# Kernel tuning notes

Measured on AMD Instinct MI355X. Metric: run time of the kernel, lower is better.

Reference implementation:

```python
import jax, jax.numpy as jnp
import numpy as np

EMBED_DIM = 1024
NUM_HEADS = 16
HEAD_DIM = EMBED_DIM // NUM_HEADS


def setup_inputs() -> dict:
    key = jax.random.key(0)
    kx, kq, kk, kv, ko = jax.random.split(key, 5)
    B, S = 4, 2048
    std = 1.0 / np.sqrt(EMBED_DIM)
    x = jax.random.normal(kx, (B, S, EMBED_DIM), dtype=jnp.float32)
    # nn.Linear weights stored as [out, in]; applied as x @ W.T
    Wq = jax.random.normal(kq, (EMBED_DIM, EMBED_DIM), dtype=jnp.float32) * std
    Wk = jax.random.normal(kk, (EMBED_DIM, EMBED_DIM), dtype=jnp.float32) * std
    Wv = jax.random.normal(kv, (EMBED_DIM, EMBED_DIM), dtype=jnp.float32) * std
    Wo = jax.random.normal(ko, (EMBED_DIM, EMBED_DIM), dtype=jnp.float32) * std
    return {"x": x, "Wq": Wq, "Wk": Wk, "Wv": Wv, "Wo": Wo}


def reference(x, Wq, Wk, Wv, Wo):
    B, S, E = x.shape
    H, D = NUM_HEADS, HEAD_DIM
    scale = jnp.sqrt(jnp.float32(D))

    def proj(W):
        # x @ W.T -> (B, S, E) -> (B, H, S, D)
        return (x @ W.T).reshape(B, S, H, D).transpose(0, 2, 1, 3)

    q, k, v = proj(Wq), proj(Wk), proj(Wv)
    scores = jnp.einsum("bhsd,bhtd->bhst", q, k) / scale  # (B,H,S,S)
    causal = jnp.tril(jnp.ones((S, S), dtype=bool))
    scores = jnp.where(causal, scores, -jnp.inf)
    attn = jax.nn.softmax(scores, axis=-1)  # dropout in eval mode = identity
    out = jnp.einsum("bhst,bhtd->bhsd", attn, v)  # (B,H,S,D)
    out = out.transpose(0, 2, 1, 3).reshape(B, S, E)
    return out @ Wo.T
```

## Files before the change

kernel.cpp:

```cpp
#include <hip/hip_runtime.h>
#include <stdint.h>

#define NHEADS 16
#define EDIM   1024
#define SEQ    2048
#define BATCH  4

typedef float  floatx4 __attribute__((ext_vector_type(4)));
typedef __bf16 bf16x8  __attribute__((ext_vector_type(8)));
typedef unsigned short u16;

__device__ __forceinline__ u16 f2bf(float f) {
  union { float f; unsigned int u; } v; v.f = f;
  return (u16)((v.u + 0x7fffu + ((v.u >> 16) & 1u)) >> 16);
}

__device__ __forceinline__ unsigned int pkbf(float lo, float hi) {
  union { float f; unsigned int u; } a, c;
  a.f = lo; c.f = hi;
  return __builtin_amdgcn_perm(c.u + 0x8000u, a.u + 0x8000u, 0x07060302u);
}

__device__ __forceinline__ void gl2lds16(const u16* g, u16* l) {
  __builtin_amdgcn_global_load_lds(
      (const __attribute__((address_space(1))) unsigned int*)g,
      (__attribute__((address_space(3))) unsigned int*)l, 16, 0, 0);
}

__global__ void cvt_all(const float* __restrict__ x,  const float* __restrict__ wq,
                        const float* __restrict__ wk, const float* __restrict__ wv,
                        const float* __restrict__ wo, u16* __restrict__ xb,
                        u16* __restrict__ wqkv, u16* __restrict__ wob, float qscale) {
  const float* src; u16* dst; int n4; float sc = 1.f;
  switch (blockIdx.y) {
    case 0: src = x;  dst = xb;             n4 = 2097152; break;
    case 1: src = wq; dst = wqkv;           n4 = 262144; sc = qscale; break;
    case 2: src = wk; dst = wqkv + 1048576; n4 = 262144; break;
    case 3: src = wv; dst = wqkv + 2097152; n4 = 262144; break;
    default: src = wo; dst = wob;           n4 = 262144; break;
  }
  const int stride = gridDim.x * blockDim.x;
  for (int i = blockIdx.x * blockDim.x + threadIdx.x; i < n4; i += stride) {
    float4 f = ((const float4*)src)[i];
    uint2 o;
    o.x = pkbf(f.x * sc, f.y * sc);
    o.y = pkbf(f.z * sc, f.w * sc);
    ((uint2*)dst)[i] = o;
  }
}

template <int MODE>
__global__ __launch_bounds__(256, 2)
void gemm_tn(const u16* __restrict__ A, const u16* __restrict__ B,
             void* __restrict__ Cq, u16* __restrict__ Ck, u16* __restrict__ Cv,
             int Kdim) {
  __shared__ u16 As[128 * 64];
  __shared__ u16 Bs[128 * 64];
  const int tid  = threadIdx.x;
  const int w    = tid >> 6, lane = tid & 63;
  const int quad = lane >> 4, l15 = lane & 15;
  const int sr   = lane >> 3, sc8 = lane & 7;
  const int rowA0 = blockIdx.y * 128, rowB0 = blockIdx.x * 128;
  const int wrow  = (w >> 1) * 64,    wcol  = (w & 1) * 64;

  const floatx4 vzero = {0.f, 0.f, 0.f, 0.f};
  floatx4 acc[4][4];
#pragma unroll
  for (int mi = 0; mi < 4; ++mi)
#pragma unroll
    for (int ni = 0; ni < 4; ++ni) acc[mi][ni] = vzero;

  for (int k0 = 0; k0 < Kdim; k0 += 64) {
    __syncthreads();
#pragma unroll
    for (int i = 0; i < 4; ++i) {
      const int r = w * 32 + i * 8;
      gl2lds16(A + (size_t)(rowA0 + r + sr) * Kdim + k0 + ((sc8 ^ sr) * 8), As + r * 64);
      gl2lds16(B + (size_t)(rowB0 + r + sr) * Kdim + k0 + ((sc8 ^ sr) * 8), Bs + r * 64);
    }
    __syncthreads();
#pragma unroll
    for (int ks = 0; ks < 2; ++ks) {
      bf16x8 af[4], bfr[4];
#pragma unroll
      for (int mi = 0; mi < 4; ++mi)
        af[mi] = *(const bf16x8*)(As + (wrow + mi * 16 + l15) * 64 + (((ks * 4 + quad) ^ (l15 & 7)) * 8));
#pragma unroll
      for (int ni = 0; ni < 4; ++ni)
        bfr[ni] = *(const bf16x8*)(Bs + (wcol + ni * 16 + l15) * 64 + (((ks * 4 + quad) ^ (l15 & 7)) * 8));
#pragma unroll
      for (int mi = 0; mi < 4; ++mi)
#pragma unroll
        for (int ni = 0; ni < 4; ++ni) {
          if (MODE == 2)
            acc[mi][ni] = __builtin_amdgcn_mfma_f32_16x16x32_bf16(bfr[ni], af[mi], acc[mi][ni], 0, 0, 0);
          else
            acc[mi][ni] = __builtin_amdgcn_mfma_f32_16x16x32_bf16(af[mi], bfr[ni], acc[mi][ni], 0, 0, 0);
        }
    }
  }

  const int matid = (MODE == 0) ? (rowA0 >> 10) : 0;
#pragma unroll
  for (int mi = 0; mi < 4; ++mi)
#pragma unroll
    for (int ni = 0; ni < 4; ++ni) {
      if (MODE == 1) {
        const int e0 = rowA0 + wrow + mi * 16 + quad * 4;
        const int s  = rowB0 + wcol + ni * 16 + l15;
        *(floatx4*)((float*)Cq + (size_t)s * 1024 + e0) = acc[mi][ni];
      } else if (MODE == 0) {
        const int e0 = rowA0 + wrow + mi * 16 + quad * 4;
        const int s  = rowB0 + wcol + ni * 16 + l15;
        const int e_loc = e0 & 1023;
        u16* dst = (matid == 0) ? (u16*)Cq : Ck;
        uint2 pk;
        pk.x = pkbf(acc[mi][ni][0], acc[mi][ni][1]);
        pk.y = pkbf(acc[mi][ni][2], acc[mi][ni][3]);
        *(uint2*)(dst + (size_t)s * 1024 + e_loc) = pk;
      } else {
        const int e_loc = rowA0 + wrow + mi * 16 + l15;
        const int s_full = rowB0 + wcol + ni * 16 + quad * 4;
        const int pos = (s_full & ~31) | (quad << 3) | ((ni & 1) << 2);
        const int bb = pos >> 11, pos_loc = pos & 2047;
        uint2 pk;
        pk.x = pkbf(acc[mi][ni][0], acc[mi][ni][1]);
        pk.y = pkbf(acc[mi][ni][2], acc[mi][ni][3]);
        *(uint2*)(Cv + (size_t)(bb * 1024 + e_loc) * SEQ + pos_loc) = pk;
      }
    }
}

__global__ __launch_bounds__(512, 4)
void attn_fwd(const u16* __restrict__ Q, const u16* __restrict__ K,
              const u16* __restrict__ Vp, u16* __restrict__ Ctx) {
  __shared__ u16 SMEM[4 * 8192];
  const int tid  = threadIdx.x;
  const int w    = tid >> 6, lane = tid & 63;
  const int quad = lane >> 4, l15 = lane & 15;
  const int qg = w >> 1, tg = w & 1;
  const int bh = blockIdx.x, b = bh >> 4, h = bh & 15;
  const int qt = 15 - (int)blockIdx.y;
  const int kmax = qt;
  const int q0 = qt * 128 + qg * 32;

  bf16x8 bq[2][2];
#pragma unroll
  for (int ni = 0; ni < 2; ++ni)
#pragma unroll
    for (int ks = 0; ks < 2; ++ks) {
      const int qs = q0 + ni * 16 + l15;
      bq[ni][ks] = *(const bf16x8*)(Q + (size_t)(b * SEQ + qs) * EDIM + h * 64 + ks * 32 + quad * 8);
    }

  const floatx4 vzero = {0.f, 0.f, 0.f, 0.f};
  floatx4 o_acc[4][2];
  float l_acc[2] = {0.f, 0.f};
#pragma unroll
  for (int di = 0; di < 4; ++di)
#pragma unroll
    for (int ni = 0; ni < 2; ++ni) o_acc[di][ni] = vzero;

  const int krow = lane >> 3, kch = lane & 7;
  const int vrow = lane >> 4, vch = lane & 15;

#define STAGE_KV(buf, ktn)                                                          \
  {                                                                                 \
    _Pragma("unroll")                                                               \
    for (int ii = 0; ii < 2; ++ii) {                                                \
      const int r0 = w * 16 + ii * 8;                                               \
      const int row = r0 + krow;                                                    \
      gl2lds16(K + (size_t)(b * SEQ + (ktn) * 128 + row) * EDIM + h * 64 +          \
                   ((kch ^ (row & 7)) * 8),                                         \
               SMEM + (buf) * 8192 + r0 * 64);                                      \
      const int d0 = w * 8 + ii * 4;                                                \
      const int dd = d0 + vrow;                                                     \
      gl2lds16(Vp + (size_t)(bh * 64 + dd) * SEQ + (ktn) * 128 +                    \
                   ((vch ^ (dd & 15)) * 8),                                         \
               SMEM + 16384 + (buf) * 8192 + d0 * 128);                             \
    }                                                                               \
  }

  STAGE_KV(0, 0);

  for (int kt = 0; kt <= kmax; ++kt) {
    const int cur = kt & 1;
    __syncthreads();
    if (kt < kmax) STAGE_KV(cur ^ 1, kt + 1);
    const u16* Ksc = SMEM + cur * 8192;
    const u16* Vsc = SMEM + 16384 + cur * 8192;

    unsigned int pk[2][2][4];
#pragma unroll
    for (int mi = 0; mi < 4; ++mi) {
      floatx4 s[2] = {vzero, vzero};
#pragma unroll
      for (int ks = 0; ks < 2; ++ks) {
        bf16x8 ak = *(const bf16x8*)(Ksc + (tg * 64 + mi * 16 + l15) * 64 +
                                     (((ks * 4 + quad) ^ (l15 & 7)) * 8));
#pragma unroll
        for (int ni = 0; ni < 2; ++ni)
          s[ni] = __builtin_amdgcn_mfma_f32_16x16x32_bf16(ak, bq[ni][ks], s[ni], 0, 0, 0);
      }
      if (kt == kmax) {
#pragma unroll
        for (int ni = 0; ni < 2; ++ni)
#pragma unroll
          for (int r = 0; r < 4; ++r) {
            const int t_loc = tg * 64 + mi * 16 + quad * 4 + r;
            const int q_loc = qg * 32 + ni * 16 + l15;
            if (t_loc > q_loc) s[ni][r] = -1e30f;
          }
      }
#pragma unroll
      for (int ni = 0; ni < 2; ++ni) {
        float p0 = __builtin_amdgcn_exp2f(s[ni][0]);
        float p1 = __builtin_amdgcn_exp2f(s[ni][1]);
        float p2 = __builtin_amdgcn_exp2f(s[ni][2]);
        float p3 = __builtin_amdgcn_exp2f(s[ni][3]);
        l_acc[ni] += (p0 + p1) + (p2 + p3);
        pk[ni][mi >> 1][(mi & 1) * 2 + 0] = pkbf(p0, p1);
        pk[ni][mi >> 1][(mi & 1) * 2 + 1] = pkbf(p2, p3);
      }
    }

#pragma unroll
    for (int ks = 0; ks < 2; ++ks) {
      bf16x8 va[4];
#pragma unroll
      for (int di = 0; di < 4; ++di)
        va[di] = *(const bf16x8*)(Vsc + (di * 16 + l15) * 128 +
                                  (((tg * 8 + ks * 4 + quad) ^ l15) * 8));
#pragma unroll
      for (int ni = 0; ni < 2; ++ni) {
        union { unsigned int u[4]; bf16x8 v; } pb;
        pb.u[0] = pk[ni][ks][0]; pb.u[1] = pk[ni][ks][1];
        pb.u[2] = pk[ni][ks][2]; pb.u[3] = pk[ni][ks][3];
#pragma unroll
        for (int di = 0; di < 4; ++di)
          o_acc[di][ni] = __builtin_amdgcn_mfma_f32_16x16x32_bf16(va[di], pb.v, o_acc[di][ni], 0, 0, 0);
      }
    }
  }

  float lt[2];
#pragma unroll
  for (int ni = 0; ni < 2; ++ni) {
    float v = l_acc[ni];
    v += __shfl_xor(v, 16, 64);
    v += __shfl_xor(v, 32, 64);
    lt[ni] = v;
  }
  __syncthreads();
  float* red  = (float*)SMEM;
  float* lred = red + 8448;
  if (tg == 1) {
#pragma unroll
    for (int ni = 0; ni < 2; ++ni) {
#pragma unroll
      for (int di = 0; di < 4; ++di)
#pragma unroll
        for (int r = 0; r < 4; ++r)
          red[qg * 2112 + (di * 16 + quad * 4 + r) * 33 + ni * 16 + l15] = o_acc[di][ni][r];
      if (quad == 0) lred[qg * 32 + ni * 16 + l15] = lt[ni];
    }
  }
  __syncthreads();
  if (tg == 0) {
#pragma unroll
    for (int ni = 0; ni < 2; ++ni) {
      const float rl = 1.f / (lt[ni] + lred[qg * 32 + ni * 16 + l15]);
      const int qs = q0 + ni * 16 + l15;
#pragma unroll
      for (int di = 0; di < 4; ++di) {
        float v0 = (o_acc[di][ni][0] + red[qg * 2112 + (di * 16 + quad * 4 + 0) * 33 + ni * 16 + l15]) * rl;
        float v1 = (o_acc[di][ni][1] + red[qg * 2112 + (di * 16 + quad * 4 + 1) * 33 + ni * 16 + l15]) * rl;
        float v2 = (o_acc[di][ni][2] + red[qg * 2112 + (di * 16 + quad * 4 + 2) * 33 + ni * 16 + l15]) * rl;
        float v3 = (o_acc[di][ni][3] + red[qg * 2112 + (di * 16 + quad * 4 + 3) * 33 + ni * 16 + l15]) * rl;
        uint2 ov;
        ov.x = pkbf(v0, v1);
        ov.y = pkbf(v2, v3);
        *(uint2*)(Ctx + (size_t)(b * SEQ + qs) * EDIM + h * 64 + di * 16 + quad * 4) = ov;
      }
    }
  }
#undef STAGE_KV
}

extern "C" void kernel_launch(void* const* d_in, const int* in_sizes, int n_in,
                              void* d_out, int out_size, void* d_ws, size_t ws_size,
                              hipStream_t stream) {
  const float* x  = (const float*)d_in[0];
  const float* Wq = (const float*)d_in[1];
  const float* Wk = (const float*)d_in[2];
  const float* Wv = (const float*)d_in[3];
  const float* Wo = (const float*)d_in[4];
  float* out = (float*)d_out;
  u16* ws = (u16*)d_ws;

  const size_t ME = (size_t)BATCH * SEQ * EDIM;
  u16* Xb   = ws;
  u16* Wqkv = Xb + ME;
  u16* Wob  = Wqkv + 3u * 1024 * 1024;
  u16* Qb   = Wob + 1024u * 1024;
  u16* Kb   = Qb + ME;
  u16* Vpb  = Kb + ME;
  u16* Ctx  = Vpb + ME;

  const float qscale = 0.125f * 1.44269504f;

  cvt_all<<<dim3(512, 5), 256, 0, stream>>>(x, Wq, Wk, Wv, Wo, Xb, Wqkv, Wob, qscale);
  gemm_tn<0><<<dim3(64, 16), 256, 0, stream>>>(Wqkv, Xb, (void*)Qb, Kb, nullptr, EDIM);
  gemm_tn<2><<<dim3(64, 8), 256, 0, stream>>>(Wqkv + 2u * 1048576, Xb, nullptr, nullptr, Vpb, EDIM);
  attn_fwd<<<dim3(64, 16), 512, 0, stream>>>(Qb, Kb, Vpb, Ctx);
  gemm_tn<1><<<dim3(64, 8), 256, 0, stream>>>(Wob, Ctx, (void*)out, nullptr, nullptr, EDIM);
}
```

Baseline: 222.8 us.

## Replace GEMMs with 256-wide tiles, 4-stage async LDS pipeline and swizzled block order

The 128x128 single-buffered GEMM is replaced by a 512-thread kernel with 256-column tiles (256 or 128 rows) and a 4-slot ring of LDS buffers. Loads run three K-steps ahead, tracked with explicit vmcnt waits and one barrier per step instead of two. The block index is remapped so neighbouring blocks share operand rows in L2, and s_setprio is raised around the MFMA bursts. This targets load latency and sync stalls in the projection GEMMs, but uses more LDS and registers per block, which can lower occupancy, and the grids are much smaller (256 blocks).

```diff
diff --git a/kernel.cpp b/kernel.cpp
--- a/kernel.cpp
+++ b/kernel.cpp
@@ -49,60 +49,110 @@
   }
 }
 
-template <int MODE>
-__global__ __launch_bounds__(256, 2)
-void gemm_tn(const u16* __restrict__ A, const u16* __restrict__ B,
+template <int MODE, int WM>
+__global__ __launch_bounds__(512, 2)
+void gemm256(const u16* __restrict__ A, const u16* __restrict__ B,
              void* __restrict__ Cq, u16* __restrict__ Ck, u16* __restrict__ Cv,
              int Kdim) {
-  __shared__ u16 As[128 * 64];
-  __shared__ u16 Bs[128 * 64];
+  constexpr int BM = WM * 32;
+  __shared__ u16 As[4][BM * 32];
+  __shared__ u16 Bs[4][256 * 32];
   const int tid  = threadIdx.x;
   const int w    = tid >> 6, lane = tid & 63;
   const int quad = lane >> 4, l15 = lane & 15;
-  const int sr   = lane >> 3, sc8 = lane & 7;
-  const int rowA0 = blockIdx.y * 128, rowB0 = blockIdx.x * 128;
-  const int wrow  = (w >> 1) * 64,    wcol  = (w & 1) * 64;
+  const int wm = w >> 2, wn = w & 3;
+  const int wrow = wm * (WM * 16), wcol = wn * 64;
+
+  const int f  = blockIdx.y * 32 + blockIdx.x;
+  const int bx = (f & 7) * 4 + ((f >> 3) & 3);
+  const int by = f >> 5;
+  const int rowA0 = by * BM, rowB0 = bx * 256;
+
+  const int rl = lane >> 2, cp = lane & 3;
+  const u16* srcA[BM / 128];
+  const u16* srcB[2];
+#pragma unroll
+  for (int ii = 0; ii < BM / 128; ++ii) {
+    const int ra = ii * 128 + w * 16 + rl;
+    srcA[ii] = A + (size_t)(rowA0 + ra) * Kdim + (cp ^ ((ra >> 1) & 3)) * 8;
+  }
+#pragma unroll
+  for (int ii = 0; ii < 2; ++ii) {
+    const int rb = ii * 128 + w * 16 + rl;
+    srcB[ii] = B + (size_t)(rowB0 + rb) * Kdim + (cp ^ ((rb >> 1) & 3)) * 8;
+  }
+
+#define STAGE256(slot, tt)                                                  \
+  {                                                                         \
+    const int kko = (tt) * 32;                                              \
+    _Pragma("unroll")                                                       \
+    for (int ii = 0; ii < BM / 128; ++ii)                                   \
+      gl2lds16(srcA[ii] + kko, (u16*)As[slot] + (ii * 128 + w * 16) * 32);  \
+    _Pragma("unroll")                                                       \
+    for (int ii = 0; ii < 2; ++ii)                                          \
+      gl2lds16(srcB[ii] + kko, (u16*)Bs[slot] + (ii * 128 + w * 16) * 32);  \
+  }
 
   const floatx4 vzero = {0.f, 0.f, 0.f, 0.f};
-  floatx4 acc[4][4];
-#pragma unroll
-  for (int mi = 0; mi < 4; ++mi)
+  floatx4 acc[WM][4];
+#pragma unroll
+  for (int mi = 0; mi < WM; ++mi)
 #pragma unroll
     for (int ni = 0; ni < 4; ++ni) acc[mi][ni] = vzero;
 
-  for (int k0 = 0; k0 < Kdim; k0 += 64) {
-    __syncthreads();
-#pragma unroll
-    for (int i = 0; i < 4; ++i) {
-      const int r = w * 32 + i * 8;
-      gl2lds16(A + (size_t)(rowA0 + r + sr) * Kdim + k0 + ((sc8 ^ sr) * 8), As + r * 64);
-      gl2lds16(B + (size_t)(rowB0 + r + sr) * Kdim + k0 + ((sc8 ^ sr) * 8), Bs + r * 64);
-    }
-    __syncthreads();
-#pragma unroll
-    for (int ks = 0; ks < 2; ++ks) {
-      bf16x8 af[4], bfr[4];
-#pragma unroll
-      for (int mi = 0; mi < 4; ++mi)
-        af[mi] = *(const bf16x8*)(As + (wrow + mi * 16 + l15) * 64 + (((ks * 4 + quad) ^ (l15 & 7)) * 8));
-#pragma unroll
-      for (int ni = 0; ni < 4; ++ni)
-        bfr[ni] = *(const bf16x8*)(Bs + (wcol + ni * 16 + l15) * 64 + (((ks * 4 + quad) ^ (l15 & 7)) * 8));
-#pragma unroll
-      for (int mi = 0; mi < 4; ++mi)
+  const int NT = Kdim >> 5;
+  STAGE256(0, 0);
+  STAGE256(1, 1);
+  STAGE256(2, 2);
+  if constexpr (WM == 8) asm volatile("s_waitcnt vmcnt(8)" ::: "memory");
+  else                   asm volatile("s_waitcnt vmcnt(6)" ::: "memory");
+  __builtin_amdgcn_s_barrier();
+
+  const int swz8 = (quad ^ ((l15 >> 1) & 3)) * 8;
+
+  for (int t = 0; t < NT; ++t) {
+    const int slot = t & 3;
+    if (t + 3 < NT) STAGE256((t + 3) & 3, t + 3);
+    const u16* Asl = As[slot];
+    const u16* Bsl = Bs[slot];
+    bf16x8 bfr[4];
+#pragma unroll
+    for (int ni = 0; ni < 4; ++ni)
+      bfr[ni] = *(const bf16x8*)(Bsl + (wcol + ni * 16 + l15) * 32 + swz8);
+#pragma unroll
+    for (int mq = 0; mq < WM / 4; ++mq) {
+      bf16x8 af[4];
+#pragma unroll
+      for (int j = 0; j < 4; ++j)
+        af[j] = *(const bf16x8*)(Asl + (wrow + (mq * 4 + j) * 16 + l15) * 32 + swz8);
+      __builtin_amdgcn_s_setprio(1);
+#pragma unroll
+      for (int j = 0; j < 4; ++j)
 #pragma unroll
         for (int ni = 0; ni < 4; ++ni) {
           if (MODE == 2)
-            acc[mi][ni] = __builtin_amdgcn_mfma_f32_16x16x32_bf16(bfr[ni], af[mi], acc[mi][ni], 0, 0, 0);
+            acc[mq * 4 + j][ni] = __builtin_amdgcn_mfma_f32_16x16x32_bf16(bfr[ni], af[j], acc[mq * 4 + j][ni], 0, 0, 0);
           else
-            acc[mi][ni] = __builtin_amdgcn_mfma_f32_16x16x32_bf16(af[mi], bfr[ni], acc[mi][ni], 0, 0, 0);
+            acc[mq * 4 + j][ni] = __builtin_amdgcn_mfma_f32_16x16x32_bf16(af[j], bfr[ni], acc[mq * 4 + j][ni], 0, 0, 0);
         }
-    }
-  }
+      __builtin_amdgcn_s_setprio(0);
+    }
+    if (t + 3 < NT) {
+      if constexpr (WM == 8) asm volatile("s_waitcnt vmcnt(8)" ::: "memory");
+      else                   asm volatile("s_waitcnt vmcnt(6)" ::: "memory");
+    } else if (t + 2 < NT) {
+      if constexpr (WM == 8) asm volatile("s_waitcnt vmcnt(4)" ::: "memory");
+      else                   asm volatile("s_waitcnt vmcnt(3)" ::: "memory");
+    } else if (t + 1 < NT) {
+      asm volatile("s_waitcnt vmcnt(0)" ::: "memory");
+    }
+    __builtin_amdgcn_s_barrier();
+  }
+#undef STAGE256
 
   const int matid = (MODE == 0) ? (rowA0 >> 10) : 0;
 #pragma unroll
-  for (int mi = 0; mi < 4; ++mi)
+  for (int mi = 0; mi < WM; ++mi)
 #pragma unroll
     for (int ni = 0; ni < 4; ++ni) {
       if (MODE == 1) {
@@ -310,8 +360,8 @@
   const float qscale = 0.125f * 1.44269504f;
 
   cvt_all<<<dim3(512, 5), 256, 0, stream>>>(x, Wq, Wk, Wv, Wo, Xb, Wqkv, Wob, qscale);
-  gemm_tn<0><<<dim3(64, 16), 256, 0, stream>>>(Wqkv, Xb, (void*)Qb, Kb, nullptr, EDIM);
-  gemm_tn<2><<<dim3(64, 8), 256, 0, stream>>>(Wqkv + 2u * 1048576, Xb, nullptr, nullptr, Vpb, EDIM);
+  gemm256<0, 8><<<dim3(32, 8), 512, 0, stream>>>(Wqkv, Xb, (void*)Qb, Kb, nullptr, EDIM);
+  gemm256<2, 4><<<dim3(32, 8), 512, 0, stream>>>(Wqkv + 2u * 1048576, Xb, nullptr, nullptr, Vpb, EDIM);
   attn_fwd<<<dim3(64, 16), 512, 0, stream>>>(Qb, Kb, Vpb, Ctx);
-  gemm_tn<1><<<dim3(64, 8), 256, 0, stream>>>(Wob, Ctx, (void*)out, nullptr, nullptr, EDIM);
-}
+  gemm256<1, 4><<<dim3(32, 8), 512, 0, stream>>>(Wob, Ctx, (void*)out, nullptr, nullptr, EDIM);
+}
```

Measured after the change: 249.7 us. 1.12x slower.

## Replace GEMM with 256x256-tile, 8-wave, double-buffered pipelined bf16 GEMM

Applied to the files above, without the earlier changes.

Replaces the 128x128, 4-wave GEMM with a 256x256-tile, 512-thread kernel. It double-buffers LDS in 32-wide K halves and interleaves async global->LDS loads with MFMA phases, using explicit barriers, waitcnt and setprio. It also remaps block indices in a grouped order to improve L2 reuse. The intent is to hide load latency and raise MFMA utilisation for the QKV and output projections. The cost is 128KB of LDS per block and fewer blocks (128-256 on the device), which may underfill the CUs.

```diff
diff --git a/kernel.cpp b/kernel.cpp
--- a/kernel.cpp
+++ b/kernel.cpp
@@ -50,68 +50,124 @@
 }
 
 template <int MODE>
-__global__ __launch_bounds__(256, 2)
-void gemm_tn(const u16* __restrict__ A, const u16* __restrict__ B,
-             void* __restrict__ Cq, u16* __restrict__ Ck, u16* __restrict__ Cv,
-             int Kdim) {
-  __shared__ u16 As[128 * 64];
-  __shared__ u16 Bs[128 * 64];
+__global__ __launch_bounds__(512, 2)
+void gemm8p(const u16* __restrict__ A, const u16* __restrict__ B,
+            void* __restrict__ Cq, u16* __restrict__ Ck, u16* __restrict__ Cv) {
+  __shared__ __align__(16) u16 LDS[65536];
   const int tid  = threadIdx.x;
   const int w    = tid >> 6, lane = tid & 63;
   const int quad = lane >> 4, l15 = lane & 15;
-  const int sr   = lane >> 3, sc8 = lane & 7;
-  const int rowA0 = blockIdx.y * 128, rowB0 = blockIdx.x * 128;
-  const int wrow  = (w >> 1) * 64,    wcol  = (w & 1) * 64;
+  const int wm = w >> 2, wn = w & 3;
+  const int arow = wm * 128, bcol = wn * 64;
+
+  const int f  = (int)blockIdx.x;
+  const int bx = (f & 7) * 4 + ((f >> 3) & 3);
+  const int by = f >> 5;
+  const int rowA0 = by * 256, rowB0 = bx * 256;
+
+  const int sr0 = w * 32 + (lane >> 2);
+  const int cp  = lane & 3;
+  const u16* srcA0 = A + (size_t)(rowA0 + sr0) * 1024 + (cp ^ ((sr0 >> 1) & 3)) * 8;
+  const u16* srcA1 = srcA0 + 16 * 1024;
+  const u16* srcB0 = B + (size_t)(rowB0 + sr0) * 1024 + (cp ^ ((sr0 >> 1) & 3)) * 8;
+  const u16* srcB1 = srcB0 + 16 * 1024;
+  const int ld0 = w * 1024, ld1 = w * 1024 + 512;
+
+#define STG_A(bufc, khc, tt)                                                 \
+  {                                                                          \
+    const int _o  = ((bufc) * 2 + (khc)) * 8192;                             \
+    const int _ko = (tt) * 64 + (khc) * 32;                                  \
+    gl2lds16(srcA0 + _ko, LDS + _o + ld0);                                   \
+    gl2lds16(srcA1 + _ko, LDS + _o + ld1);                                   \
+  }
+#define STG_B(bufc, khc, tt)                                                 \
+  {                                                                          \
+    const int _o  = 32768 + ((bufc) * 2 + (khc)) * 8192;                     \
+    const int _ko = (tt) * 64 + (khc) * 32;                                  \
+    gl2lds16(srcB0 + _ko, LDS + _o + ld0);                                   \
+    gl2lds16(srcB1 + _ko, LDS + _o + ld1);                                   \
+  }
 
   const floatx4 vzero = {0.f, 0.f, 0.f, 0.f};
-  floatx4 acc[4][4];
-#pragma unroll
-  for (int mi = 0; mi < 4; ++mi)
+  floatx4 acc[8][4];
+#pragma unroll
+  for (int mi = 0; mi < 8; ++mi)
 #pragma unroll
     for (int ni = 0; ni < 4; ++ni) acc[mi][ni] = vzero;
-
-  for (int k0 = 0; k0 < Kdim; k0 += 64) {
-    __syncthreads();
-#pragma unroll
-    for (int i = 0; i < 4; ++i) {
-      const int r = w * 32 + i * 8;
-      gl2lds16(A + (size_t)(rowA0 + r + sr) * Kdim + k0 + ((sc8 ^ sr) * 8), As + r * 64);
-      gl2lds16(B + (size_t)(rowB0 + r + sr) * Kdim + k0 + ((sc8 ^ sr) * 8), Bs + r * 64);
-    }
-    __syncthreads();
-#pragma unroll
-    for (int ks = 0; ks < 2; ++ks) {
-      bf16x8 af[4], bfr[4];
-#pragma unroll
-      for (int mi = 0; mi < 4; ++mi)
-        af[mi] = *(const bf16x8*)(As + (wrow + mi * 16 + l15) * 64 + (((ks * 4 + quad) ^ (l15 & 7)) * 8));
-#pragma unroll
-      for (int ni = 0; ni < 4; ++ni)
-        bfr[ni] = *(const bf16x8*)(Bs + (wcol + ni * 16 + l15) * 64 + (((ks * 4 + quad) ^ (l15 & 7)) * 8));
-#pragma unroll
-      for (int mi = 0; mi < 4; ++mi)
-#pragma unroll
-        for (int ni = 0; ni < 4; ++ni) {
-          if (MODE == 2)
-            acc[mi][ni] = __builtin_amdgcn_mfma_f32_16x16x32_bf16(bfr[ni], af[mi], acc[mi][ni], 0, 0, 0);
-          else
-            acc[mi][ni] = __builtin_amdgcn_mfma_f32_16x16x32_bf16(af[mi], bfr[ni], acc[mi][ni], 0, 0, 0);
-        }
-    }
-  }
+  bf16x8 bk[2][4];
+  const int swz8 = (quad ^ ((l15 >> 1) & 3)) * 8;
+
+#define PHASE(bufc, khc, msub, STAGE, CKPT)                                  \
+  {                                                                          \
+    bf16x8 af[4];                                                            \
+    const u16* _ra = LDS + ((bufc) * 2 + (khc)) * 8192 +                     \
+                     (arow + (msub) * 64 + l15) * 32 + swz8;                 \
+    _Pragma("unroll")                                                        \
+    for (int j = 0; j < 4; ++j) af[j] = *(const bf16x8*)(_ra + j * 512);     \
+    if ((msub) == 0) {                                                       \
+      const u16* _rb = LDS + 32768 + ((bufc) * 2 + (khc)) * 8192 +           \
+                       (bcol + l15) * 32 + swz8;                             \
+      _Pragma("unroll")                                                      \
+      for (int nj = 0; nj < 4; ++nj)                                         \
+        bk[khc][nj] = *(const bf16x8*)(_rb + nj * 512);                      \
+    }                                                                        \
+    STAGE;                                                                   \
+    CKPT;                                                                    \
+    __builtin_amdgcn_s_barrier();                                            \
+    asm volatile("s_waitcnt lgkmcnt(0)" ::: "memory");                       \
+    __builtin_amdgcn_sched_barrier(0);                                       \
+    __builtin_amdgcn_s_setprio(1);                                           \
+    _Pragma("unroll")                                                        \
+    for (int j = 0; j < 4; ++j)                                              \
+      _Pragma("unroll")                                                      \
+      for (int nj = 0; nj < 4; ++nj) {                                       \
+        if (MODE == 2)                                                       \
+          acc[(msub) * 4 + j][nj] = __builtin_amdgcn_mfma_f32_16x16x32_bf16( \
+              bk[khc][nj], af[j], acc[(msub) * 4 + j][nj], 0, 0, 0);         \
+        else                                                                 \
+          acc[(msub) * 4 + j][nj] = __builtin_amdgcn_mfma_f32_16x16x32_bf16( \
+              af[j], bk[khc][nj], acc[(msub) * 4 + j][nj], 0, 0, 0);         \
+      }                                                                      \
+    __builtin_amdgcn_s_setprio(0);                                           \
+    __builtin_amdgcn_s_barrier();                                            \
+  }
+
+  STG_B(0, 0, 0); STG_B(0, 1, 0); STG_A(0, 0, 0); STG_A(0, 1, 0);
+  STG_B(1, 0, 1); STG_B(1, 1, 1); STG_A(1, 0, 1);
+  asm volatile("s_waitcnt vmcnt(6)" ::: "memory");
+  __builtin_amdgcn_s_barrier();
+
+  for (int i = 0; i < 8; ++i) {
+    const int t1 = 2 * i + 1, t2 = 2 * i + 2, t3 = 2 * i + 3;
+    const bool g = (i < 7);
+    PHASE(0, 0, 0, { STG_A(1, 1, t1); }, {});
+    PHASE(0, 1, 0, { if (g) STG_B(0, 0, t2); }, {});
+    PHASE(0, 0, 1, { if (g) STG_B(0, 1, t2); }, {});
+    PHASE(0, 1, 1, { if (g) STG_A(0, 0, t2); },
+          { if (g) { asm volatile("s_waitcnt vmcnt(6)" ::: "memory"); }
+            else   { asm volatile("s_waitcnt vmcnt(0)" ::: "memory"); } });
+    PHASE(1, 0, 0, { if (g) STG_A(0, 1, t2); }, {});
+    PHASE(1, 1, 0, { if (g) STG_B(1, 0, t3); }, {});
+    PHASE(1, 0, 1, { if (g) STG_B(1, 1, t3); }, {});
+    PHASE(1, 1, 1, { if (g) STG_A(1, 0, t3); },
+          { if (g) { asm volatile("s_waitcnt vmcnt(6)" ::: "memory"); } });
+  }
+#undef PHASE
+#undef STG_A
+#undef STG_B
 
   const int matid = (MODE == 0) ? (rowA0 >> 10) : 0;
 #pragma unroll
-  for (int mi = 0; mi < 4; ++mi)
+  for (int mi = 0; mi < 8; ++mi)
 #pragma unroll
     for (int ni = 0; ni < 4; ++ni) {
       if (MODE == 1) {
-        const int e0 = rowA0 + wrow + mi * 16 + quad * 4;
-        const int s  = rowB0 + wcol + ni * 16 + l15;
+        const int e0 = rowA0 + arow + mi * 16 + quad * 4;
+        const int s  = rowB0 + bcol + ni * 16 + l15;
         *(floatx4*)((float*)Cq + (size_t)s * 1024 + e0) = acc[mi][ni];
       } else if (MODE == 0) {
-        const int e0 = rowA0 + wrow + mi * 16 + quad * 4;
-        const int s  = rowB0 + wcol + ni * 16 + l15;
+        const int e0 = rowA0 + arow + mi * 16 + quad * 4;
+        const int s  = rowB0 + bcol + ni * 16 + l15;
         const int e_loc = e0 & 1023;
         u16* dst = (matid == 0) ? (u16*)Cq : Ck;
         uint2 pk;
@@ -119,8 +175,8 @@
         pk.y = pkbf(acc[mi][ni][2], acc[mi][ni][3]);
         *(uint2*)(dst + (size_t)s * 1024 + e_loc) = pk;
       } else {
-        const int e_loc = rowA0 + wrow + mi * 16 + l15;
-        const int s_full = rowB0 + wcol + ni * 16 + quad * 4;
+        const int e_loc = rowA0 + arow + mi * 16 + l15;
+        const int s_full = rowB0 + bcol + ni * 16 + quad * 4;
         const int pos = (s_full & ~31) | (quad << 3) | ((ni & 1) << 2);
         const int bb = pos >> 11, pos_loc = pos & 2047;
         uint2 pk;
@@ -310,8 +366,8 @@
   const float qscale = 0.125f * 1.44269504f;
 
   cvt_all<<<dim3(512, 5), 256, 0, stream>>>(x, Wq, Wk, Wv, Wo, Xb, Wqkv, Wob, qscale);
-  gemm_tn<0><<<dim3(64, 16), 256, 0, stream>>>(Wqkv, Xb, (void*)Qb, Kb, nullptr, EDIM);
-  gemm_tn<2><<<dim3(64, 8), 256, 0, stream>>>(Wqkv + 2u * 1048576, Xb, nullptr, nullptr, Vpb, EDIM);
+  gemm8p<0><<<dim3(256), 512, 0, stream>>>(Wqkv, Xb, (void*)Qb, Kb, nullptr);
+  gemm8p<2><<<dim3(128), 512, 0, stream>>>(Wqkv + 2u * 1048576, Xb, nullptr, nullptr, Vpb);
   attn_fwd<<<dim3(64, 16), 512, 0, stream>>>(Qb, Kb, Vpb, Ctx);
-  gemm_tn<1><<<dim3(64, 8), 256, 0, stream>>>(Wob, Ctx, (void*)out, nullptr, nullptr, EDIM);
-}
+  gemm8p<1><<<dim3(128), 512, 0, stream>>>(Wob, Ctx, (void*)out, nullptr, nullptr);
+}
```

Result: slower. 241.1 us (+8.2%).

## Replace GEMM with triple-buffered 512-thread pipelined kernel and grouped tile swizzle

Applied to the files above, without the earlier changes.

Rewrites the projection GEMMs as a 512-thread kernel with a 3-slot LDS ring of K=32 slices. Global-to-LDS loads for step t+2 are issued while step t computes, and a single barrier per step uses vmcnt waits. It also remaps block indices into grouped tiles to improve L2 reuse, uses a wider 256-column tile for the QK projection, and raises MFMA priority with setprio. The aim is to hide memory latency that the old load-sync-compute loop exposed, at the cost of more complex waitcnt logic and higher LDS and register pressure.

```diff
diff --git a/kernel.cpp b/kernel.cpp
--- a/kernel.cpp
+++ b/kernel.cpp
@@ -49,69 +49,103 @@
   }
 }
 
-template <int MODE>
-__global__ __launch_bounds__(256, 2)
-void gemm_tn(const u16* __restrict__ A, const u16* __restrict__ B,
-             void* __restrict__ Cq, u16* __restrict__ Ck, u16* __restrict__ Cv,
-             int Kdim) {
-  __shared__ u16 As[128 * 64];
-  __shared__ u16 Bs[128 * 64];
+template <int MODE, int BN, int GBX>
+__global__ __launch_bounds__(512, 4)
+void gemm_r3(const u16* __restrict__ A, const u16* __restrict__ B,
+             void* __restrict__ Cq, u16* __restrict__ Ck, u16* __restrict__ Cv) {
+  constexpr int NI   = BN / 64;
+  constexpr int SLOT = (128 + BN) * 32;
+  constexpr int BOFF = 128 * 32;
+  __shared__ __align__(16) u16 ring[3][SLOT];
   const int tid  = threadIdx.x;
   const int w    = tid >> 6, lane = tid & 63;
   const int quad = lane >> 4, l15 = lane & 15;
-  const int sr   = lane >> 3, sc8 = lane & 7;
-  const int rowA0 = blockIdx.y * 128, rowB0 = blockIdx.x * 128;
-  const int wrow  = (w >> 1) * 64,    wcol  = (w & 1) * 64;
+  const int wrow = (w >> 2) * 64, bcol = (w & 3) * (BN / 4);
+
+  const int f  = (int)blockIdx.x;
+  const int g  = f >> 3;
+  const int bx = (f & 7) * GBX + (g % GBX);
+  const int by = g / GBX;
+  const int rowA0 = by * 128, rowB0 = bx * BN;
+
+  const int cp = lane & 3;
+  const int ra = w * 16 + (lane >> 2);
+  const u16* srcA = A + (size_t)(rowA0 + ra) * 1024 + (cp ^ ((ra >> 1) & 3)) * 8;
+  const int rb0 = (BN == 256) ? (w * 32 + (lane >> 2)) : (w * 16 + (lane >> 2));
+  const u16* srcB0 = B + (size_t)(rowB0 + rb0) * 1024 + (cp ^ ((rb0 >> 1) & 3)) * 8;
+  const u16* srcB1 = srcB0 + 16 * 1024;
+
+#define STG(sl, tt)                                                          \
+  {                                                                          \
+    const int _ko = (tt) * 32;                                               \
+    gl2lds16(srcA + _ko, &ring[sl][0] + w * 512);                            \
+    if (BN == 256) {                                                         \
+      gl2lds16(srcB0 + _ko, &ring[sl][BOFF] + w * 1024);                     \
+      gl2lds16(srcB1 + _ko, &ring[sl][BOFF] + w * 1024 + 512);               \
+    } else {                                                                 \
+      gl2lds16(srcB0 + _ko, &ring[sl][BOFF] + w * 512);                      \
+    }                                                                        \
+  }
 
   const floatx4 vzero = {0.f, 0.f, 0.f, 0.f};
-  floatx4 acc[4][4];
+  floatx4 acc[4][NI];
 #pragma unroll
   for (int mi = 0; mi < 4; ++mi)
 #pragma unroll
-    for (int ni = 0; ni < 4; ++ni) acc[mi][ni] = vzero;
-
-  for (int k0 = 0; k0 < Kdim; k0 += 64) {
-    __syncthreads();
-#pragma unroll
-    for (int i = 0; i < 4; ++i) {
-      const int r = w * 32 + i * 8;
-      gl2lds16(A + (size_t)(rowA0 + r + sr) * Kdim + k0 + ((sc8 ^ sr) * 8), As + r * 64);
-      gl2lds16(B + (size_t)(rowB0 + r + sr) * Kdim + k0 + ((sc8 ^ sr) * 8), Bs + r * 64);
-    }
-    __syncthreads();
-#pragma unroll
-    for (int ks = 0; ks < 2; ++ks) {
-      bf16x8 af[4], bfr[4];
-#pragma unroll
-      for (int mi = 0; mi < 4; ++mi)
-        af[mi] = *(const bf16x8*)(As + (wrow + mi * 16 + l15) * 64 + (((ks * 4 + quad) ^ (l15 & 7)) * 8));
-#pragma unroll
-      for (int ni = 0; ni < 4; ++ni)
-        bfr[ni] = *(const bf16x8*)(Bs + (wcol + ni * 16 + l15) * 64 + (((ks * 4 + quad) ^ (l15 & 7)) * 8));
-#pragma unroll
-      for (int mi = 0; mi < 4; ++mi)
-#pragma unroll
-        for (int ni = 0; ni < 4; ++ni) {
-          if (MODE == 2)
-            acc[mi][ni] = __builtin_amdgcn_mfma_f32_16x16x32_bf16(bfr[ni], af[mi], acc[mi][ni], 0, 0, 0);
-          else
-            acc[mi][ni] = __builtin_amdgcn_mfma_f32_16x16x32_bf16(af[mi], bfr[ni], acc[mi][ni], 0, 0, 0);
-        }
-    }
-  }
+    for (int ni = 0; ni < NI; ++ni) acc[mi][ni] = vzero;
+
+  const int swz8 = (quad ^ ((l15 >> 1) & 3)) * 8;
+  constexpr int NT = 32;
+  STG(0, 0);
+  STG(1, 1);
+  int cs = 0, ss = 2;
+
+  for (int t = 0; t < NT; ++t) {
+    if (t < NT - 1) {
+      if constexpr (BN == 256) asm volatile("s_waitcnt vmcnt(3)" ::: "memory");
+      else                     asm volatile("s_waitcnt vmcnt(2)" ::: "memory");
+    } else {
+      asm volatile("s_waitcnt vmcnt(0)" ::: "memory");
+    }
+    __builtin_amdgcn_s_barrier();
+    if (t + 2 < NT) { STG(ss, t + 2); ss = (ss == 2) ? 0 : ss + 1; }
+
+    const u16* As = &ring[cs][0];
+    const u16* Bs = &ring[cs][BOFF];
+    cs = (cs == 2) ? 0 : cs + 1;
+    bf16x8 af[4], bfr[NI];
+#pragma unroll
+    for (int j = 0; j < 4; ++j)
+      af[j] = *(const bf16x8*)(As + (wrow + j * 16 + l15) * 32 + swz8);
+#pragma unroll
+    for (int nj = 0; nj < NI; ++nj)
+      bfr[nj] = *(const bf16x8*)(Bs + (bcol + nj * 16 + l15) * 32 + swz8);
+    __builtin_amdgcn_s_setprio(1);
+#pragma unroll
+    for (int mi = 0; mi < 4; ++mi)
+#pragma unroll
+      for (int ni = 0; ni < NI; ++ni) {
+        if (MODE == 2)
+          acc[mi][ni] = __builtin_amdgcn_mfma_f32_16x16x32_bf16(bfr[ni], af[mi], acc[mi][ni], 0, 0, 0);
+        else
+          acc[mi][ni] = __builtin_amdgcn_mfma_f32_16x16x32_bf16(af[mi], bfr[ni], acc[mi][ni], 0, 0, 0);
+      }
+    __builtin_amdgcn_s_setprio(0);
+  }
+#undef STG
 
   const int matid = (MODE == 0) ? (rowA0 >> 10) : 0;
 #pragma unroll
   for (int mi = 0; mi < 4; ++mi)
 #pragma unroll
-    for (int ni = 0; ni < 4; ++ni) {
+    for (int ni = 0; ni < NI; ++ni) {
       if (MODE == 1) {
         const int e0 = rowA0 + wrow + mi * 16 + quad * 4;
-        const int s  = rowB0 + wcol + ni * 16 + l15;
+        const int s  = rowB0 + bcol + ni * 16 + l15;
         *(floatx4*)((float*)Cq + (size_t)s * 1024 + e0) = acc[mi][ni];
       } else if (MODE == 0) {
         const int e0 = rowA0 + wrow + mi * 16 + quad * 4;
-        const int s  = rowB0 + wcol + ni * 16 + l15;
+        const int s  = rowB0 + bcol + ni * 16 + l15;
         const int e_loc = e0 & 1023;
         u16* dst = (matid == 0) ? (u16*)Cq : Ck;
         uint2 pk;
@@ -120,7 +154,7 @@
         *(uint2*)(dst + (size_t)s * 1024 + e_loc) = pk;
       } else {
         const int e_loc = rowA0 + wrow + mi * 16 + l15;
-        const int s_full = rowB0 + wcol + ni * 16 + quad * 4;
+        const int s_full = rowB0 + bcol + ni * 16 + quad * 4;
         const int pos = (s_full & ~31) | (quad << 3) | ((ni & 1) << 2);
         const int bb = pos >> 11, pos_loc = pos & 2047;
         uint2 pk;
@@ -310,8 +344,8 @@
   const float qscale = 0.125f * 1.44269504f;
 
   cvt_all<<<dim3(512, 5), 256, 0, stream>>>(x, Wq, Wk, Wv, Wo, Xb, Wqkv, Wob, qscale);
-  gemm_tn<0><<<dim3(64, 16), 256, 0, stream>>>(Wqkv, Xb, (void*)Qb, Kb, nullptr, EDIM);
-  gemm_tn<2><<<dim3(64, 8), 256, 0, stream>>>(Wqkv + 2u * 1048576, Xb, nullptr, nullptr, Vpb, EDIM);
+  gemm_r3<0, 256, 4><<<dim3(512), 512, 0, stream>>>(Wqkv, Xb, (void*)Qb, Kb, nullptr);
+  gemm_r3<2, 128, 8><<<dim3(512), 512, 0, stream>>>(Wqkv + 2u * 1048576, Xb, nullptr, nullptr, Vpb);
   attn_fwd<<<dim3(64, 16), 512, 0, stream>>>(Qb, Kb, Vpb, Ctx);
-  gemm_tn<1><<<dim3(64, 8), 256, 0, stream>>>(Wob, Ctx, (void*)out, nullptr, nullptr, EDIM);
-}
+  gemm_r3<1, 128, 8><<<dim3(512), 512, 0, stream>>>(Wob, Ctx, (void*)out, nullptr, nullptr);
+}
```

Result: slower. 240.2 us (+7.8%).
